# Kernel tuning notes

Measured on AMD Instinct MI355X. Metric: run time of the kernel, lower is better.

Reference implementation:

```python
import jax, jax.numpy as jnp
import numpy as np
from jax import lax

VOCAB = 400000
D = 300          # embedding_dim
L = 2000         # seq len
B = 4            # batch
C1, K1 = 64, 3   # conv1 outChan, kernel
C2, K2 = 128, 500
HID = 256
NCLS = 5


def setup_inputs() -> dict:
    key = jax.random.key(0)
    ks = jax.random.split(key, 8)
    x = jax.random.randint(ks[0], (B, L), 0, VOCAB)
    emb_table = jax.random.normal(ks[1], (VOCAB, D), jnp.float32) * 0.1
    conv1_w = jax.random.normal(ks[2], (C1, 1, K1), jnp.float32) * 0.1
    conv1_b = jnp.zeros((C1,), jnp.float32)
    conv2_w = jax.random.normal(ks[3], (C2, C1, K2), jnp.float32) * 0.02
    conv2_b = jnp.zeros((C2,), jnp.float32)
    lin1_w = jax.random.normal(ks[4], (HID, C2), jnp.float32) * 0.05
    lin1_b = jnp.zeros((HID,), jnp.float32)
    lin2_w = jax.random.normal(ks[5], (NCLS, HID), jnp.float32) * 0.05
    lin2_b = jnp.zeros((NCLS,), jnp.float32)
    return dict(x=x, emb_table=emb_table,
                conv1_w=conv1_w, conv1_b=conv1_b,
                conv2_w=conv2_w, conv2_b=conv2_b,
                lin1_w=lin1_w, lin1_b=lin1_b,
                lin2_w=lin2_w, lin2_b=lin2_b)


def _conv1d(x, w):
    # x: [N, Cin, W]; w: [Cout, Cin, K]; VALID, stride 1
    return lax.conv_general_dilated(x, w, window_strides=(1,), padding='VALID',
                                    dimension_numbers=('NCH', 'OIH', 'NCH'))


def _maxpool1d(x, k):
    # kernel == stride (torch MaxPool1d default)
    return lax.reduce_window(x, -jnp.inf, lax.max, (1, 1, k), (1, 1, k), 'VALID')


def reference(x, emb_table, conv1_w, conv1_b, conv2_w, conv2_b,
              lin1_w, lin1_b, lin2_w, lin2_b):
    emb = emb_table[x]                                  # [B, L, D]
    # concat module == reshape to [B, 1, L*D]
    out = emb.reshape(emb.shape[0], 1, emb.shape[1] * emb.shape[2])
    out = _conv1d(out, conv1_w) + conv1_b[None, :, None]  # [B, C1, L*D-K1+1]
    out = _maxpool1d(jax.nn.relu(out), D)                 # pool 300
    out = _conv1d(out, conv2_w) + conv2_b[None, :, None]  # [B, C2, 1500]
    out = _maxpool1d(jax.nn.relu(out), D * 5)             # pool 1500 -> len 1
    out = out.reshape(out.shape[0], -1)                   # [B, C2]
    out = jax.nn.relu(out @ lin1_w.T + lin1_b)            # [B, HID]
    out = jax.nn.softmax(out @ lin2_w.T + lin2_b, axis=-1)  # [B, 5]
    # Dropout is identity in eval mode
    return out
```

## Files before the change

kernel.cpp:

```cpp
#include <hip/hip_runtime.h>
#include <hip/hip_bf16.h>
#include <math.h>

#define VOCAB 400000
#define D     300
#define L     2000
#define B     4
#define C1    64
#define C2    128
#define K2    500
#define HID   256
#define NCLS  5
#define NP1   1999
#define T2    1500
#define TPAD  2304
#define S     8
#define CI    8
#define NK2   125
#define BN    192
#define NKT   1600
#define NC1B  (B * 500)

typedef __attribute__((ext_vector_type(8))) short short8v;
typedef __attribute__((ext_vector_type(4))) float f32x4;

__device__ __forceinline__ void gload_lds16(const void* g, void* l) {
    __builtin_amdgcn_global_load_lds(
        (const __attribute__((address_space(1))) void*)g,
        (__attribute__((address_space(3))) void*)l, 16, 0, 0);
}

__global__ __launch_bounds__(256) void k_prep(
    const int* __restrict__ x, const float* __restrict__ emb,
    const float* __restrict__ w1, const float* __restrict__ b1,
    const float* __restrict__ w2,
    __hip_bfloat16* __restrict__ in1T, __hip_bfloat16* __restrict__ aT)
{
    __shared__ float smem[2560];
    int bid = blockIdx.x, tid = threadIdx.x;
    if (bid < NKT) {
        int s  = bid / 200;
        int rem = bid % 200;
        int kc = rem / 8, cog = rem % 8;
        int co0 = cog * 16;
        for (int i = tid; i < 2560; i += 256) {
            int co_l = i / 160, r = i % 160, ci = r / 20, kl = r % 20;
            smem[i] = w2[((size_t)(co0 + co_l) * C1 + s * CI + ci) * K2 + kc * 20 + kl];
        }
        __syncthreads();
        for (int u = tid; u < 320; u += 256) {
            int co_l = u & 15, gk = u >> 4;
            int g = gk & 3, k2l = gk >> 2;
            __hip_bfloat16 tmp[8];
#pragma unroll
            for (int e = 0; e < 8; ++e)
                tmp[e] = __float2bfloat16(smem[co_l * 160 + e * 20 + 4 * k2l + g]);
            size_t off = ((size_t)((s * NK2 + kc * 5 + k2l) * 4 + g)) * 1024
                       + (size_t)(co0 + co_l) * 8;
            *reinterpret_cast<int4*>(aT + off) = *reinterpret_cast<const int4*>(tmp);
        }
    } else {
        int blk = bid - NKT;
        int b = blk / 500, pb = blk % 500;
        int p0 = pb * 4;
        float* sig = smem;
        if (tid < 301) {
            int rj = tid / 75, col = (tid % 75) * 4;
            int xi = p0 + rj; if (xi > L - 1) xi = L - 1;
            int row = x[b * L + xi];
            *reinterpret_cast<float4*>(sig + 4 * tid) =
                *reinterpret_cast<const float4*>(emb + (size_t)row * D + col);
        }
        __syncthreads();
        int c = tid & 63, pg = tid >> 6;
        int p = p0 + pg;
        float wa = w1[c * 3 + 0], wb = w1[c * 3 + 1], wc = w1[c * 3 + 2];
        float bb = b1[c];
        int jb = 300 * pg;
        float m = -INFINITY;
        float4 cur = *reinterpret_cast<float4*>(sig + jb);
        for (int st = 0; st < 75; ++st) {
            float4 nxt = *reinterpret_cast<float4*>(sig + jb + 4 * st + 4);
            float xx[8] = {cur.x, cur.y, cur.z, cur.w, nxt.x, nxt.y, nxt.z, nxt.w};
#pragma unroll
            for (int q = 0; q < 4; ++q) {
                float v = fmaf(wc, xx[q + 2], fmaf(wb, xx[q + 1], fmaf(wa, xx[q], bb)));
                m = fmaxf(m, v);
            }
            cur = nxt;
        }
        if (p < NP1) {
            int sg = c >> 3, ci = c & 7;
            in1T[((size_t)(b * S + sg) * TPAD + p) * CI + ci] =
                __float2bfloat16(fmaxf(m, 0.0f));
        }
    }
}

__global__ __launch_bounds__(512, 1) void k2_mfma(
    const __hip_bfloat16* __restrict__ in1T,
    const __hip_bfloat16* __restrict__ aT,
    float* __restrict__ part)
{
    int bid = blockIdx.x;
    int s = bid & 7;
    int rem = bid >> 3;
    int b = rem >> 3, ti = rem & 7;
    int t0 = ti * BN;

    __shared__ __align__(16) __hip_bfloat16 seg[768 * CI];

    int tid = threadIdx.x;
    int w = tid >> 6, l = tid & 63;
    int lane16 = l & 15, g = l >> 4;
    int co0w = (w & 1) * 64;
    int tn0  = (w >> 1) * 48;

    {
        const char* gsrc = (const char*)(in1T + ((size_t)(b * S + s) * TPAD + t0) * CI);
        char* lb = (char*)seg + w * 1024;
        gload_lds16(gsrc + (size_t)tid * 16, lb);
        if (tid < 256)
            gload_lds16(gsrc + (size_t)(512 + tid) * 16, lb + 8192);
    }
    __syncthreads();

    const __hip_bfloat16* abase =
        aT + (size_t)s * NK2 * 4096 + g * 1024 + (co0w + lane16) * 8;

    f32x4 acc[4][3];
#pragma unroll
    for (int fa = 0; fa < 4; ++fa)
#pragma unroll
        for (int fb = 0; fb < 3; ++fb) acc[fa][fb] = (f32x4){0.f, 0.f, 0.f, 0.f};

#define LOADA(AR, KK)                                                         \
    {                                                                         \
        _Pragma("unroll")                                                     \
        for (int fa = 0; fa < 4; ++fa)                                        \
            AR[fa] = *reinterpret_cast<const short8v*>(                       \
                abase + (size_t)(KK) * 4096 + fa * 128);                      \
    }

#define STEP(AR, KK)                                                          \
    {                                                                         \
        short8v bfr[3];                                                       \
        _Pragma("unroll")                                                     \
        for (int fb = 0; fb < 3; ++fb)                                        \
            bfr[fb] = *reinterpret_cast<const short8v*>(                      \
                seg + (size_t)(tn0 + fb * 16 + lane16 + 4 * (KK) + g) * 8);   \
        _Pragma("unroll")                                                     \
        for (int fa = 0; fa < 4; ++fa) {                                      \
            _Pragma("unroll")                                                 \
            for (int fb = 0; fb < 3; ++fb)                                    \
                acc[fa][fb] = __builtin_amdgcn_mfma_f32_16x16x32_bf16(        \
                    AR[fa], bfr[fb], acc[fa][fb], 0, 0, 0);                   \
        }                                                                     \
    }

    short8v a0[4], a1[4];
    LOADA(a0, 0);
    LOADA(a1, 1);
    int k2 = 0;
#pragma unroll 1
    for (; k2 + 3 < NK2; k2 += 2) {
        STEP(a0, k2);
        LOADA(a0, k2 + 2);
        STEP(a1, k2 + 1);
        LOADA(a1, k2 + 3);
    }
    STEP(a0, k2);
    LOADA(a0, k2 + 2);
    STEP(a1, k2 + 1);
    STEP(a0, k2 + 2);

#undef LOADA
#undef STEP

#pragma unroll
    for (int fa = 0; fa < 4; ++fa) {
#pragma unroll
        for (int fb = 0; fb < 3; ++fb) {
            int t = t0 + tn0 + fb * 16 + lane16;
            if (t < T2) {
                int cob = co0w + fa * 16 + 4 * g;
#pragma unroll
                for (int r = 0; r < 4; ++r)
                    part[((size_t)(s * B + b) * C2 + cob + r) * T2 + t] =
                        acc[fa][fb][r];
            }
        }
    }
}

__global__ __launch_bounds__(256) void k2b_pool(
    const float* __restrict__ part, const float* __restrict__ b2,
    float* __restrict__ h1)
{
    int bc = blockIdx.x;
    int b = bc / C2, co = bc % C2;
    int tid = threadIdx.x;
    float m = -INFINITY;
    for (int t4 = tid; t4 < T2 / 4; t4 += 256) {
        float4 sum = {0.f, 0.f, 0.f, 0.f};
#pragma unroll
        for (int s = 0; s < S; ++s) {
            const float4* p = reinterpret_cast<const float4*>(
                part + ((size_t)(s * B + b) * C2 + co) * T2);
            float4 v = p[t4];
            sum.x += v.x; sum.y += v.y; sum.z += v.z; sum.w += v.w;
        }
        m = fmaxf(m, fmaxf(fmaxf(sum.x, sum.y), fmaxf(sum.z, sum.w)));
    }
    __shared__ float red[256];
    red[tid] = m;
    __syncthreads();
    for (int st = 128; st > 0; st >>= 1) {
        if (tid < st) red[tid] = fmaxf(red[tid], red[tid + st]);
        __syncthreads();
    }
    if (tid == 0) h1[bc] = fmaxf(red[0] + b2[co], 0.0f);
}

__global__ __launch_bounds__(256) void k3_head(
    const float* __restrict__ h1,
    const float* __restrict__ wl1, const float* __restrict__ bl1,
    const float* __restrict__ wl2, const float* __restrict__ bl2,
    float* __restrict__ out)
{
    int b = blockIdx.x;
    int tid = threadIdx.x;
    __shared__ float xin[C2];
    __shared__ float hbuf[HID];
    __shared__ float lg[NCLS];
    if (tid < C2) xin[tid] = h1[b * C2 + tid];
    __syncthreads();
    float a = bl1[tid];
    for (int c = 0; c < C2; ++c) a = fmaf(xin[c], wl1[tid * C2 + c], a);
    hbuf[tid] = fmaxf(a, 0.0f);
    __syncthreads();
    if (tid < NCLS) {
        float lv = bl2[tid];
        for (int j = 0; j < HID; ++j) lv = fmaf(hbuf[j], wl2[tid * HID + j], lv);
        lg[tid] = lv;
    }
    __syncthreads();
    if (tid < NCLS) {
        float mx = lg[0];
        for (int i = 1; i < NCLS; ++i) mx = fmaxf(mx, lg[i]);
        float sum = 0.f;
        for (int i = 0; i < NCLS; ++i) sum += expf(lg[i] - mx);
        out[b * NCLS + tid] = expf(lg[tid] - mx) / sum;
    }
}

extern "C" void kernel_launch(void* const* d_in, const int* in_sizes, int n_in,
                              void* d_out, int out_size, void* d_ws, size_t ws_size,
                              hipStream_t stream)
{
    const int*   x   = (const int*)  d_in[0];
    const float* emb = (const float*)d_in[1];
    const float* w1  = (const float*)d_in[2];
    const float* b1  = (const float*)d_in[3];
    const float* w2  = (const float*)d_in[4];
    const float* b2  = (const float*)d_in[5];
    const float* wl1 = (const float*)d_in[6];
    const float* bl1 = (const float*)d_in[7];
    const float* wl2 = (const float*)d_in[8];
    const float* bl2 = (const float*)d_in[9];
    float* out = (float*)d_out;

    float* ws   = (float*)d_ws;
    float* part = ws;
    float* h1   = ws + (size_t)S * B * C2 * T2;
    __hip_bfloat16* in1T = (__hip_bfloat16*)(h1 + 512);
    __hip_bfloat16* aT   = in1T + (size_t)B * S * TPAD * CI;

    hipLaunchKernelGGL(k_prep, dim3(NKT + NC1B), dim3(256), 0, stream,
                       x, emb, w1, b1, w2, in1T, aT);
    hipLaunchKernelGGL(k2_mfma, dim3(256), dim3(512), 0, stream, in1T, aT, part);
    hipLaunchKernelGGL(k2b_pool, dim3(B * C2), dim3(256), 0, stream, part, b2, h1);
    hipLaunchKernelGGL(k3_head, dim3(B), dim3(256), 0, stream,
                       h1, wl1, bl1, wl2, bl2, out);
}
```

Measured before the change: 82.76 us.

## Halve conv2 MFMA tile to 256-thread blocks and simplify weight repack

The conv2 MFMA kernel now uses 96-column time tiles with 256-thread blocks. That doubles the grid to 512 blocks and allows two blocks per CU, improving occupancy and CU balance. The cost is reloading a 640-row input segment per tile, so input reuse per block drops. The weight repack in the prep kernel shrinks from 1600 shared-memory-staged blocks to 128 blocks that read w2 directly. Those direct reads are strided and uncoalesced, which may slow the prep phase.

```diff
diff --git a/kernel.cpp b/kernel.cpp
--- a/kernel.cpp
+++ b/kernel.cpp
@@ -17,8 +17,9 @@
 #define S     8
 #define CI    8
 #define NK2   125
-#define BN    192
-#define NKT   1600
+#define BN    96
+#define SEGR  640
+#define NWT   128
 #define NC1B  (B * 500)
 
 typedef __attribute__((ext_vector_type(8))) short short8v;
@@ -36,31 +37,25 @@
     const float* __restrict__ w2,
     __hip_bfloat16* __restrict__ in1T, __hip_bfloat16* __restrict__ aT)
 {
-    __shared__ float smem[2560];
+    __shared__ float smem[1204];
     int bid = blockIdx.x, tid = threadIdx.x;
-    if (bid < NKT) {
-        int s  = bid / 200;
-        int rem = bid % 200;
-        int kc = rem / 8, cog = rem % 8;
-        int co0 = cog * 16;
-        for (int i = tid; i < 2560; i += 256) {
-            int co_l = i / 160, r = i % 160, ci = r / 20, kl = r % 20;
-            smem[i] = w2[((size_t)(co0 + co_l) * C1 + s * CI + ci) * K2 + kc * 20 + kl];
-        }
-        __syncthreads();
-        for (int u = tid; u < 320; u += 256) {
-            int co_l = u & 15, gk = u >> 4;
-            int g = gk & 3, k2l = gk >> 2;
+    if (bid < NWT) {
+        int s = bid >> 4, cog = bid & 15;
+        for (int u = tid; u < 4000; u += 256) {
+            int co_l = u & 7, kg = u >> 3;
+            int k2 = kg >> 2, g = kg & 3;
+            int co = cog * 8 + co_l;
             __hip_bfloat16 tmp[8];
 #pragma unroll
             for (int e = 0; e < 8; ++e)
-                tmp[e] = __float2bfloat16(smem[co_l * 160 + e * 20 + 4 * k2l + g]);
-            size_t off = ((size_t)((s * NK2 + kc * 5 + k2l) * 4 + g)) * 1024
-                       + (size_t)(co0 + co_l) * 8;
-            *reinterpret_cast<int4*>(aT + off) = *reinterpret_cast<const int4*>(tmp);
+                tmp[e] = __float2bfloat16(
+                    w2[((size_t)co * C1 + s * CI + e) * K2 + 4 * k2 + g]);
+            *reinterpret_cast<int4*>(
+                aT + ((size_t)((s * NK2 + k2) * 4 + g)) * 1024 + (size_t)co * 8) =
+                *reinterpret_cast<const int4*>(tmp);
         }
     } else {
-        int blk = bid - NKT;
+        int blk = bid - NWT;
         int b = blk / 500, pb = blk % 500;
         int p0 = pb * 4;
         float* sig = smem;
@@ -97,7 +92,7 @@
     }
 }
 
-__global__ __launch_bounds__(512, 1) void k2_mfma(
+__global__ __launch_bounds__(256, 2) void k2_mfma(
     const __hip_bfloat16* __restrict__ in1T,
     const __hip_bfloat16* __restrict__ aT,
     float* __restrict__ part)
@@ -105,10 +100,10 @@
     int bid = blockIdx.x;
     int s = bid & 7;
     int rem = bid >> 3;
-    int b = rem >> 3, ti = rem & 7;
+    int b = rem >> 4, ti = rem & 15;
     int t0 = ti * BN;
 
-    __shared__ __align__(16) __hip_bfloat16 seg[768 * CI];
+    __shared__ __align__(16) __hip_bfloat16 seg[SEGR * CI];
 
     int tid = threadIdx.x;
     int w = tid >> 6, l = tid & 63;
@@ -120,7 +115,8 @@
         const char* gsrc = (const char*)(in1T + ((size_t)(b * S + s) * TPAD + t0) * CI);
         char* lb = (char*)seg + w * 1024;
         gload_lds16(gsrc + (size_t)tid * 16, lb);
-        if (tid < 256)
+        gload_lds16(gsrc + (size_t)(256 + tid) * 16, lb + 4096);
+        if (tid < 128)
             gload_lds16(gsrc + (size_t)(512 + tid) * 16, lb + 8192);
     }
     __syncthreads();
@@ -142,7 +138,7 @@
                 abase + (size_t)(KK) * 4096 + fa * 128);                      \
     }
 
-#define STEP(AR, KK)                                                          \
+#define STEP(AR, KK)                                                         \
     {                                                                         \
         short8v bfr[3];                                                       \
         _Pragma("unroll")                                                     \
@@ -276,9 +272,9 @@
     __hip_bfloat16* in1T = (__hip_bfloat16*)(h1 + 512);
     __hip_bfloat16* aT   = in1T + (size_t)B * S * TPAD * CI;
 
-    hipLaunchKernelGGL(k_prep, dim3(NKT + NC1B), dim3(256), 0, stream,
+    hipLaunchKernelGGL(k_prep, dim3(NWT + NC1B), dim3(256), 0, stream,
                        x, emb, w1, b1, w2, in1T, aT);
-    hipLaunchKernelGGL(k2_mfma, dim3(256), dim3(512), 0, stream, in1T, aT, part);
+    hipLaunchKernelGGL(k2_mfma, dim3(512), dim3(256), 0, stream, in1T, aT, part);
     hipLaunchKernelGGL(k2b_pool, dim3(B * C2), dim3(256), 0, stream, part, b2, h1);
     hipLaunchKernelGGL(k3_head, dim3(B), dim3(256), 0, stream,
                        h1, wl1, bl1, wl2, bl2, out);
```

New measurement: 78.78 us. -4.8%, faster.
